# Kernel tuning notes

Hardware: AMD Instinct MI355X
Metric: run time of the kernel (lower is better)

The kernel has to match this reference:

```python
import jax, jax.numpy as jnp
import numpy as np

N = 100000   # nodes
E = 1600000  # edges
D = 128      # feature dim
G = 64       # graphs in batch


def setup_inputs() -> dict:
    key = jax.random.key(0)
    k1, k2, k3, k4, k5, k6, k7, k8 = jax.random.split(key, 8)
    in_feat = jax.random.normal(k1, (N, D), dtype=jnp.float32)
    src = jax.random.randint(k2, (E,), 0, N, dtype=jnp.int32)
    dst = jax.random.randint(k3, (E,), 0, N, dtype=jnp.int32)
    graph_ids = jax.random.randint(k4, (N,), 0, G, dtype=jnp.int32)
    s = 1.0 / np.sqrt(D)
    W1 = jax.random.uniform(k5, (D, D), jnp.float32, -s, s)
    b1 = jnp.zeros((D,), jnp.float32)
    W2 = jax.random.uniform(k6, (D, D), jnp.float32, -s, s)
    b2 = jnp.zeros((D,), jnp.float32)
    return {"in_feat": in_feat, "W1": W1, "b1": b1, "W2": W2, "b2": b2,
            "src": src, "dst": dst, "graph_ids": graph_ids}


def _graph_conv(x, src, dst, W, b, norm_src, norm_dst):
    # DGL GraphConv, norm='both': D_out^{-1/2} A D_in^{-1/2} X W + b
    m = (x * norm_src[:, None])[src]                       # [E, d] gather
    agg = jax.ops.segment_sum(m, dst, num_segments=N)      # [N, d] scatter-add
    return (agg * norm_dst[:, None]) @ W + b


def reference(in_feat, W1, b1, W2, b2, src, dst, graph_ids):
    ones_e = jnp.ones((E,), jnp.float32)
    deg_out = jax.ops.segment_sum(ones_e, src, num_segments=N)
    deg_in = jax.ops.segment_sum(ones_e, dst, num_segments=N)
    norm_src = jnp.where(deg_out > 0, deg_out, 1.0) ** -0.5  # D_out^{-1/2}
    norm_dst = jnp.where(deg_in > 0, deg_in, 1.0) ** -0.5    # D_in^{-1/2}

    h = _graph_conv(in_feat, src, dst, W1, b1, norm_src, norm_dst)
    h = jax.nn.relu(h)
    h = _graph_conv(h, src, dst, W2, b2, norm_src, norm_dst)

    # AvgPooling: per-graph mean over nodes -> [G, D]
    sums = jax.ops.segment_sum(h, graph_ids, num_segments=G)
    counts = jax.ops.segment_sum(jnp.ones((N,), jnp.float32), graph_ids, num_segments=G)
    return sums / jnp.maximum(counts, 1.0)[:, None]
```

## Files before the change

### kernel.cpp

```cpp
#include <hip/hip_runtime.h>
#include <cstdint>


#define DD 128
#define PB 512
#define GB 384
#define KC 32
#define CHK 3200

typedef __attribute__((ext_vector_type(8))) short bf16x8;
typedef __attribute__((ext_vector_type(4))) float f32x4;
typedef __attribute__((ext_vector_type(2))) float f32x2;

__device__ __forceinline__ unsigned short f2bf(float f) {
  union { float f; unsigned u; } v; v.f = f;
  unsigned r = (v.u + 0x7fff + ((v.u >> 16) & 1)) >> 16;
  return (unsigned short)r;
}
__device__ __forceinline__ float bfhi(unsigned u) {
  union { unsigned u; float f; } v; v.u = u & 0xffff0000u; return v.f;
}
__device__ __forceinline__ float bflo(unsigned u) {
  union { unsigned u; float f; } v; v.u = u << 16; return v.f;
}
__device__ __forceinline__ unsigned char f2fp8(float f) {
  return (unsigned char)(__builtin_amdgcn_cvt_pk_fp8_f32(f, f, 0, false) & 0xff);
}

__global__ __launch_bounds__(256) void k_part1a(const int* __restrict__ src, const int* __restrict__ dst,
                                                const int* __restrict__ gid,
                                                unsigned* __restrict__ histD, unsigned* __restrict__ histS,
                                                int* __restrict__ gcnt, int E, int N, int G) {
  __shared__ unsigned hD[256], hS[256];
  __shared__ int h64[64];
  hD[threadIdx.x] = 0; hS[threadIdx.x] = 0;
  if (threadIdx.x < 64) h64[threadIdx.x] = 0;
  __syncthreads();
  int chunk = (E + gridDim.x - 1) / gridDim.x;
  int e0 = blockIdx.x * chunk, e1 = min(E, e0 + chunk);
  for (int e = e0 + threadIdx.x; e < e1; e += 256) {
    atomicAdd(&hD[(unsigned)dst[e] >> 9], 1u);
    atomicAdd(&hS[(unsigned)src[e] >> 9], 1u);
  }
  int stride = gridDim.x * 256;
  for (int i = blockIdx.x * 256 + threadIdx.x; i < N; i += stride)
    atomicAdd(&h64[gid[i]], 1);
  __syncthreads();
  histD[blockIdx.x * 256 + threadIdx.x] = hD[threadIdx.x];
  histS[blockIdx.x * 256 + threadIdx.x] = hS[threadIdx.x];
  if (threadIdx.x < (unsigned)G) {
    int v = h64[threadIdx.x];
    if (v) atomicAdd(&gcnt[threadIdx.x], v);
  }
}

__global__ __launch_bounds__(256) void k_pscanA(unsigned* __restrict__ histD, unsigned* __restrict__ histS,
                                                unsigned* __restrict__ tot) {
  __shared__ unsigned excl[PB], psc[256];
  int table = blockIdx.x >> 8, b = blockIdx.x & 255;
  unsigned* hist = table ? histS : histD;
  int t = threadIdx.x;
  unsigned s0 = hist[(2 * t) * 256 + b];
  unsigned s1 = hist[(2 * t + 1) * 256 + b];
  unsigned pr = s0 + s1;
  psc[t] = pr;
  __syncthreads();
  for (int off = 1; off < 256; off <<= 1) {
    unsigned x = (t >= off) ? psc[t - off] : 0;
    __syncthreads();
    psc[t] += x;
    __syncthreads();
  }
  unsigned pex = psc[t] - pr;
  excl[2 * t] = pex;
  excl[2 * t + 1] = pex + s0;
  __syncthreads();
  hist[(2 * t) * 256 + b] = excl[2 * t];
  hist[(2 * t + 1) * 256 + b] = excl[2 * t + 1];
  if (t == 255) tot[table * 256 + b] = psc[255];
}

__global__ __launch_bounds__(256) void k_pscanB(const unsigned* __restrict__ tot,
                                                int* __restrict__ bsD, int* __restrict__ bsS) {
  __shared__ unsigned s[256];
  int t = threadIdx.x;
#pragma unroll
  for (int table = 0; table < 2; ++table) {
    int* bs = table ? bsS : bsD;
    unsigned v = tot[table * 256 + t];
    s[t] = v;
    __syncthreads();
    for (int off = 1; off < 256; off <<= 1) {
      unsigned x = (t >= off) ? s[t - off] : 0;
      __syncthreads();
      s[t] += x;
      __syncthreads();
    }
    bs[t] = (int)(s[t] - v);
    if (t == 255) bs[256] = (int)s[255];
    __syncthreads();
  }
}

__global__ __launch_bounds__(256) void k_pscanC(unsigned* __restrict__ histD, unsigned* __restrict__ histS,
                                                const int* __restrict__ bsD, const int* __restrict__ bsS) {
  int table = blockIdx.x >> 9, i = blockIdx.x & (PB - 1);
  unsigned* hist = table ? histS : histD;
  const int* bs = table ? bsS : bsD;
  hist[i * 256 + threadIdx.x] += (unsigned)bs[threadIdx.x];
}

__global__ __launch_bounds__(256) void k_part1c(const int* __restrict__ src, const int* __restrict__ dst,
                                                const unsigned* __restrict__ histD, const unsigned* __restrict__ histS,
                                                unsigned* __restrict__ pairD, unsigned* __restrict__ pairS, int E) {
  __shared__ unsigned pk[CHK];
  __shared__ unsigned char bk[CHK];
  __shared__ unsigned hist[256], cur[256], gbase[256], psc[256];
  int chunk = (E + gridDim.x - 1) / gridDim.x;
  int e0 = blockIdx.x * chunk, e1 = min(E, e0 + chunk);
  int n = e1 - e0;
  int t = threadIdx.x;
#pragma unroll
  for (int table = 0; table < 2; ++table) {
    const unsigned* gcur = (table ? histS : histD) + blockIdx.x * 256;
    unsigned* out = table ? pairS : pairD;
    hist[t] = 0;
    __syncthreads();
    for (int i = t; i < n; i += 256) {
      unsigned key = (unsigned)(table ? src[e0 + i] : dst[e0 + i]);
      atomicAdd(&hist[key >> 9], 1u);
    }
    __syncthreads();
    unsigned v = hist[t];
    psc[t] = v;
    __syncthreads();
    for (int off = 1; off < 256; off <<= 1) {
      unsigned x = (t >= off) ? psc[t - off] : 0;
      __syncthreads();
      psc[t] += x;
      __syncthreads();
    }
    unsigned excl = psc[t] - v;
    cur[t] = excl;
    gbase[t] = gcur[t] - excl;
    __syncthreads();
    for (int i = t; i < n; i += 256) {
      unsigned sv = (unsigned)src[e0 + i], dv = (unsigned)dst[e0 + i];
      unsigned key = table ? sv : dv;
      unsigned val = table ? (((sv & 511u) << 17) | dv) : (((dv & 511u) << 17) | sv);
      unsigned b = key >> 9;
      unsigned p = atomicAdd(&cur[b], 1u);
      pk[p] = val;
      bk[p] = (unsigned char)b;
    }
    __syncthreads();
    for (int i = t; i < n; i += 256)
      out[gbase[bk[i]] + i] = pk[i];
    __syncthreads();
  }
}

__global__ __launch_bounds__(256) void k_part2d(const unsigned* __restrict__ pairD, const int* __restrict__ bsD,
                                                int* __restrict__ offs, int* __restrict__ degI,
                                                int* __restrict__ srcS, int N) {
  __shared__ unsigned hist[512], excl[512], psc[256];
  int k = blockIdx.x, base = k << 9;
  int b0 = bsD[k], b1 = bsD[k + 1];
  hist[threadIdx.x] = 0; hist[threadIdx.x + 256] = 0;
  __syncthreads();
  for (int i = b0 + threadIdx.x; i < b1; i += 256)
    atomicAdd(&hist[pairD[i] >> 17], 1u);
  __syncthreads();
  unsigned s0 = hist[2 * threadIdx.x], s1 = hist[2 * threadIdx.x + 1];
  unsigned pr = s0 + s1;
  psc[threadIdx.x] = pr;
  __syncthreads();
  for (int off = 1; off < 256; off <<= 1) {
    unsigned x = (threadIdx.x >= off) ? psc[threadIdx.x - off] : 0;
    __syncthreads();
    psc[threadIdx.x] += x;
    __syncthreads();
  }
  unsigned pex = psc[threadIdx.x] - pr;
  excl[2 * threadIdx.x] = pex;
  excl[2 * threadIdx.x + 1] = pex + s0;
  __syncthreads();
  for (int j = threadIdx.x; j < 512; j += 256) {
    int node = base + j;
    if (node <= N) offs[node] = b0 + (int)excl[j];
    if (node < N) degI[node] = (int)hist[j];
  }
  __syncthreads();
  for (int i = b0 + threadIdx.x; i < b1; i += 256) {
    unsigned pkv = pairD[i];
    unsigned pos = atomicAdd(&excl[pkv >> 17], 1u);
    srcS[b0 + (int)pos] = (int)(pkv & 0x1FFFFu);
  }
}

__global__ __launch_bounds__(256) void k_norm(const int* __restrict__ degI, const int* __restrict__ gcnt,
                                              const int* __restrict__ gid,
                                              float* __restrict__ ndst, uint2* __restrict__ pwg, int N) {
  int i = blockIdx.x * blockDim.x + threadIdx.x;
  if (i >= N) return;
  float gi = (float)degI[i]; gi = gi > 0.f ? gi : 1.f;
  float nd = rsqrtf(gi);
  ndst[i] = nd;
  float c = (float)gcnt[gid[i]]; c = c > 1.f ? c : 1.f;
  float w = nd / c;
  union { float f; unsigned u; } v; v.f = w;
  pwg[i] = make_uint2(v.u, (unsigned)gid[i]);
}

__global__ __launch_bounds__(1024, 1) void k_pw(const unsigned* __restrict__ pairS, const int* __restrict__ bsS,
                                                const uint2* __restrict__ pwg,
                                                unsigned short* __restrict__ P16,
                                                float* __restrict__ nsrc, int N) {
  __shared__ float tile[512 * 64];
  __shared__ unsigned hist[512];
  int k = blockIdx.x, base = k << 9;
  int b0 = bsS[k], b1 = bsS[k + 1];
  for (int i = threadIdx.x; i < 512 * 64; i += 1024) tile[i] = 0.f;
  if (threadIdx.x < 512) hist[threadIdx.x] = 0;
  __syncthreads();
  for (int i = b0 + threadIdx.x; i < b1; i += 1024) {
    unsigned pkv = pairS[i];
    unsigned dv = pkv & 0x1FFFFu;
    unsigned sloc = pkv >> 17;
    atomicAdd(&hist[sloc], 1u);
    uint2 u = pwg[dv];
    union { unsigned u; float f; } w; w.u = u.x;
    atomicAdd(&tile[sloc * 64 + u.y], w.f);
  }
  __syncthreads();
  if (threadIdx.x < 512) {
    int node = base + threadIdx.x;
    if (node < N) {
      float g = (float)hist[threadIdx.x]; g = g > 0.f ? g : 1.f;
      nsrc[node] = rsqrtf(g);
    }
  }
  for (int grp = threadIdx.x; grp < 4096; grp += 1024) {
    int qb = grp >> 6, g = grp & 63;
    unsigned w0 = (unsigned)f2bf(tile[(qb * 8 + 0) * 64 + g]) | ((unsigned)f2bf(tile[(qb * 8 + 1) * 64 + g]) << 16);
    unsigned w1 = (unsigned)f2bf(tile[(qb * 8 + 2) * 64 + g]) | ((unsigned)f2bf(tile[(qb * 8 + 3) * 64 + g]) << 16);
    unsigned w2 = (unsigned)f2bf(tile[(qb * 8 + 4) * 64 + g]) | ((unsigned)f2bf(tile[(qb * 8 + 5) * 64 + g]) << 16);
    unsigned w3 = (unsigned)f2bf(tile[(qb * 8 + 6) * 64 + g]) | ((unsigned)f2bf(tile[(qb * 8 + 7) * 64 + g]) << 16);
    uint4 o = make_uint4(w0, w1, w2, w3);
    *(uint4*)(P16 + ((size_t)(base >> 3) + qb) * 512 + g * 8) = o;
  }
}

__global__ __launch_bounds__(128) void k_wprep(const float* __restrict__ W, unsigned short* __restrict__ Wt) {
  int n = blockIdx.x, k = threadIdx.x;
  Wt[n * 128 + k] = f2bf(W[k * 128 + n]);
}

__global__ __launch_bounds__(256) void k_gemm1(const float* __restrict__ X, const unsigned short* __restrict__ Wt,
                                               const float* __restrict__ nsrc,
                                               unsigned char* __restrict__ Z8, int N) {
  int wave = threadIdx.x >> 6, lane = threadIdx.x & 63;
  int quad = lane >> 4, l16 = lane & 15;
  int row0 = blockIdx.x * 64 + wave * 16;
  int arow = row0 + l16; if (arow >= N) arow = N - 1;
  const float* xr = X + (size_t)arow * 128 + quad * 8;
  f32x4 acc[8];
#pragma unroll
  for (int i = 0; i < 8; ++i) acc[i] = (f32x4){0.f, 0.f, 0.f, 0.f};
#pragma unroll
  for (int kb = 0; kb < 128; kb += 32) {
    float4 x0 = *(const float4*)(xr + kb);
    float4 x1 = *(const float4*)(xr + kb + 4);
    bf16x8 a;
    a[0] = (short)f2bf(x0.x); a[1] = (short)f2bf(x0.y);
    a[2] = (short)f2bf(x0.z); a[3] = (short)f2bf(x0.w);
    a[4] = (short)f2bf(x1.x); a[5] = (short)f2bf(x1.y);
    a[6] = (short)f2bf(x1.z); a[7] = (short)f2bf(x1.w);
#pragma unroll
    for (int nt = 0; nt < 8; ++nt) {
      bf16x8 b = *(const bf16x8*)(Wt + (size_t)(nt * 16 + l16) * 128 + kb + quad * 8);
      acc[nt] = __builtin_amdgcn_mfma_f32_16x16x32_bf16(a, b, acc[nt], 0, 0, 0);
    }
  }
  int rbase = row0 + quad * 4;
#pragma unroll
  for (int r = 0; r < 4; ++r) {
    int row = rbase + r;
    if (row < N) {
      float s = nsrc[row];
#pragma unroll
      for (int nt = 0; nt < 8; ++nt)
        Z8[(size_t)row * 128 + nt * 16 + l16] = f2fp8(acc[nt][r] * s);
    }
  }
}

__global__ __launch_bounds__(256) void k_layer1(const unsigned char* __restrict__ Z8,
                                                const int* __restrict__ offs, const int* __restrict__ srcS,
                                                const float* __restrict__ b1,
                                                const float* __restrict__ nsrc, const float* __restrict__ ndst,
                                                unsigned short* __restrict__ Hb, int N) {
  int lane = threadIdx.x & 63;
  int half = lane >> 5, l32 = lane & 31;
  int d = blockIdx.x * 4 + (threadIdx.x >> 6);
  if (d >= N) return;
  int start = offs[d], end = offs[d + 1];
  float a0 = 0.f, a1 = 0.f, a2 = 0.f, a3 = 0.f;
  int e = start;
  for (; e + 8 <= end; e += 8) {
    int s0 = srcS[e + half], s1 = srcS[e + 2 + half];
    int s2 = srcS[e + 4 + half], s3 = srcS[e + 6 + half];
    unsigned u0 = *(const unsigned*)(Z8 + (size_t)s0 * 128 + l32 * 4);
    unsigned u1 = *(const unsigned*)(Z8 + (size_t)s1 * 128 + l32 * 4);
    unsigned u2 = *(const unsigned*)(Z8 + (size_t)s2 * 128 + l32 * 4);
    unsigned u3 = *(const unsigned*)(Z8 + (size_t)s3 * 128 + l32 * 4);
    f32x2 p0 = __builtin_amdgcn_cvt_pk_f32_fp8(u0, false), q0 = __builtin_amdgcn_cvt_pk_f32_fp8(u0, true);
    f32x2 p1 = __builtin_amdgcn_cvt_pk_f32_fp8(u1, false), q1 = __builtin_amdgcn_cvt_pk_f32_fp8(u1, true);
    f32x2 p2 = __builtin_amdgcn_cvt_pk_f32_fp8(u2, false), q2 = __builtin_amdgcn_cvt_pk_f32_fp8(u2, true);
    f32x2 p3 = __builtin_amdgcn_cvt_pk_f32_fp8(u3, false), q3 = __builtin_amdgcn_cvt_pk_f32_fp8(u3, true);
    a0 += (p0[0] + p1[0]) + (p2[0] + p3[0]);
    a1 += (p0[1] + p1[1]) + (p2[1] + p3[1]);
    a2 += (q0[0] + q1[0]) + (q2[0] + q3[0]);
    a3 += (q0[1] + q1[1]) + (q2[1] + q3[1]);
  }
  for (; e + 2 <= end; e += 2) {
    int s = srcS[e + half];
    unsigned u = *(const unsigned*)(Z8 + (size_t)s * 128 + l32 * 4);
    f32x2 p = __builtin_amdgcn_cvt_pk_f32_fp8(u, false), q = __builtin_amdgcn_cvt_pk_f32_fp8(u, true);
    a0 += p[0]; a1 += p[1]; a2 += q[0]; a3 += q[1];
  }
  if (e < end && half == 0) {
    int s = srcS[e];
    unsigned u = *(const unsigned*)(Z8 + (size_t)s * 128 + l32 * 4);
    f32x2 p = __builtin_amdgcn_cvt_pk_f32_fp8(u, false), q = __builtin_amdgcn_cvt_pk_f32_fp8(u, true);
    a0 += p[0]; a1 += p[1]; a2 += q[0]; a3 += q[1];
  }
  a0 += __shfl_xor(a0, 32, 64);
  a1 += __shfl_xor(a1, 32, 64);
  a2 += __shfl_xor(a2, 32, 64);
  a3 += __shfl_xor(a3, 32, 64);
  if (half == 0) {
    float nd = ndst[d], ns = nsrc[d];
    int f = l32 * 4;
    float h0 = fmaxf(fmaf(nd, a0, b1[f + 0]), 0.f) * ns;
    float h1 = fmaxf(fmaf(nd, a1, b1[f + 1]), 0.f) * ns;
    float h2 = fmaxf(fmaf(nd, a2, b1[f + 2]), 0.f) * ns;
    float h3 = fmaxf(fmaf(nd, a3, b1[f + 3]), 0.f) * ns;
    ushort4 o; o.x = f2bf(h0); o.y = f2bf(h1); o.z = f2bf(h2); o.w = f2bf(h3);
    *(ushort4*)(Hb + (size_t)d * 128 + f) = o;
  }
}

__global__ __launch_bounds__(256) void k_poolgemm(const unsigned short* __restrict__ P16,
                                                  const unsigned short* __restrict__ Hb,
                                                  float* __restrict__ part, int N, int Kpad, int chunk) {
  __shared__ unsigned short Hl[KC * 128];
  int t = threadIdx.x;
  int r0 = blockIdx.x * chunk;
  int r1 = min(Kpad, r0 + chunk);
  int wv = t >> 6, lane = t & 63, quad = lane >> 4, l16 = lane & 15;
  f32x4 acc[8];
#pragma unroll
  for (int i = 0; i < 8; ++i) acc[i] = (f32x4){0.f, 0.f, 0.f, 0.f};
  for (int rb = r0; rb < r1; rb += KC) {
    int r = t >> 3, c = (t & 7) * 16;
    int cs = c ^ ((r >> 3) * 16);
    int row = rb + r;
    if (row < N) {
      const uint4* srcp = (const uint4*)(Hb + (size_t)row * 128 + c);
      *(uint4*)(Hl + r * 128 + cs) = srcp[0];
      *(uint4*)(Hl + r * 128 + cs + 8) = srcp[1];
    } else {
      uint4 z = make_uint4(0, 0, 0, 0);
      *(uint4*)(Hl + r * 128 + cs) = z;
      *(uint4*)(Hl + r * 128 + cs + 8) = z;
    }
    __syncthreads();
    bf16x8 a = *(const bf16x8*)(P16 + ((size_t)(rb >> 3) + quad) * 512 + (wv * 16 + l16) * 8);
#pragma unroll
    for (int ft = 0; ft < 8; ++ft) {
      bf16x8 b;
#pragma unroll
      for (int j = 0; j < 8; ++j) {
        int rr = quad * 8 + j;
        b[j] = (short)Hl[rr * 128 + ((ft ^ (rr >> 3)) * 16) + l16];
      }
      acc[ft] = __builtin_amdgcn_mfma_f32_16x16x32_bf16(a, b, acc[ft], 0, 0, 0);
    }
    __syncthreads();
  }
  float* bp = part + (size_t)blockIdx.x * 64 * DD;
#pragma unroll
  for (int ft = 0; ft < 8; ++ft)
#pragma unroll
    for (int rg = 0; rg < 4; ++rg)
      bp[(wv * 16 + quad * 4 + rg) * DD + ft * 16 + l16] = acc[ft][rg];
}

__global__ __launch_bounds__(256) void k_fold(const float* __restrict__ part, float* __restrict__ pooled) {
  int tid = blockIdx.x * 256 + threadIdx.x;
  int o = tid & 8191, grp = tid >> 13;
  float s = 0.f;
  for (int k = grp; k < GB; k += 8) s += part[(size_t)k * 8192 + o];
  unsafeAtomicAdd(&pooled[o], s);
}

__global__ __launch_bounds__(128) void k_out(const float* __restrict__ pooled, const float* __restrict__ W2,
                                             const float* __restrict__ b2, float* __restrict__ out) {
  __shared__ float p[DD];
  int g = blockIdx.x, d = threadIdx.x;
  p[d] = pooled[g * DD + d];
  __syncthreads();
  float a = b2[d];
#pragma unroll 4
  for (int k = 0; k < DD; ++k) a = fmaf(p[k], W2[k * DD + d], a);
  out[g * DD + d] = a;
}

extern "C" void kernel_launch(void* const* d_in, const int* in_sizes, int n_in,
                              void* d_out, int out_size, void* d_ws, size_t ws_size,
                              hipStream_t stream) {
  const float* X  = (const float*)d_in[0];
  const float* W1 = (const float*)d_in[1];
  const float* b1 = (const float*)d_in[2];
  const float* W2 = (const float*)d_in[3];
  const float* b2 = (const float*)d_in[4];
  const int* src  = (const int*)d_in[5];
  const int* dst  = (const int*)d_in[6];
  const int* gid  = (const int*)d_in[7];
  int E = in_sizes[5];
  int N = in_sizes[7];
  int G = out_size / DD;
  int nb = (N >> 9) + 1;
  int Kpad = nb << 9;
  int chunk = ((Kpad + GB * KC - 1) / (GB * KC)) * KC;

  char* w = (char*)d_ws;
  size_t o = 0;
  auto carve = [&](size_t bytes) { char* p = w + o; o += (bytes + 255) & ~(size_t)255; return p; };
  int*   gcnt   = (int*)  carve((size_t)G * 4);
  float* pooled = (float*)carve((size_t)G * DD * 4);
  size_t zeroBytes = o;
  unsigned* histD = (unsigned*)carve((size_t)PB * 256 * 4);
  unsigned* histS = (unsigned*)carve((size_t)PB * 256 * 4);
  unsigned* tot   = (unsigned*)carve(512 * 4);
  int*   bsD    = (int*)  carve(257 * 4);
  int*   bsS    = (int*)  carve(257 * 4);
  unsigned* pairD = (unsigned*)carve((size_t)E * 4);
  unsigned* pairS = (unsigned*)carve((size_t)E * 4);
  int*   srcS   = (int*)  carve((size_t)E * 4);
  int*   offs   = (int*)  carve((size_t)(N + 1) * 4);
  int*   degI   = (int*)  carve((size_t)N * 4);
  float* nsrc   = (float*)carve((size_t)N * 4);
  float* ndst   = (float*)carve((size_t)N * 4);
  uint2* pwg    = (uint2*)carve((size_t)N * 8);
  unsigned short* Wt = (unsigned short*)carve(128 * 128 * 2);
  unsigned char*  Z8 = (unsigned char*)carve((size_t)N * DD);
  unsigned short* Hb = (unsigned short*)carve((size_t)N * DD * 2);
  unsigned short* P16 = (unsigned short*)carve((size_t)Kpad * 64 * 2);
  float* part   = (float*)pairD;

  hipMemsetAsync(d_ws, 0, zeroBytes, stream);

  k_part1a<<<PB, 256, 0, stream>>>(src, dst, gid, histD, histS, gcnt, E, N, G);
  k_pscanA<<<512, 256, 0, stream>>>(histD, histS, tot);
  k_pscanB<<<1, 256, 0, stream>>>(tot, bsD, bsS);
  k_pscanC<<<2 * PB, 256, 0, stream>>>(histD, histS, bsD, bsS);
  k_part1c<<<PB, 256, 0, stream>>>(src, dst, histD, histS, pairD, pairS, E);
  k_part2d<<<nb, 256, 0, stream>>>(pairD, bsD, offs, degI, srcS, N);
  k_norm<<<(N + 255) / 256, 256, 0, stream>>>(degI, gcnt, gid, ndst, pwg, N);
  k_pw<<<nb, 1024, 0, stream>>>(pairS, bsS, pwg, P16, nsrc, N);
  k_wprep<<<128, 128, 0, stream>>>(W1, Wt);
  k_gemm1<<<(N + 63) / 64, 256, 0, stream>>>(X, Wt, nsrc, Z8, N);
  k_layer1<<<(N + 3) / 4, 256, 0, stream>>>(Z8, offs, srcS, b1, nsrc, ndst, Hb, N);
  k_poolgemm<<<GB, 256, 0, stream>>>(P16, Hb, part, N, Kpad, chunk);
  k_fold<<<256, 256, 0, stream>>>(part, pooled);
  k_out<<<G, DD, 0, stream>>>(pooled, W2, b2, (float*)d_out);
}
```

Measured before the change: 312.9 us.

## Map four destination nodes per wavefront with 8-byte gathers in layer-1 aggregation

The layer-1 aggregation kernel now gives each 16-lane quarter-wave its own destination node, and each lane loads 8 fp8 features (uint2) per neighbor. Before, one node used a whole wave split into two halves and ended with a cross-half shuffle reduction. Source indices for the next pair of edges are prefetched while the current pair is accumulated, with packed f32x2 accumulators. This removes idle lanes on low-degree nodes and the shuffle step, but nodes of different degree now share a wave, which adds divergence through the __any loop.

```diff
diff --git a/kernel.cpp b/kernel.cpp
--- a/kernel.cpp
+++ b/kernel.cpp
@@ -295,59 +295,63 @@
   }
 }
 
+#define ACCP(u) do {                                              \
+    c0 += __builtin_amdgcn_cvt_pk_f32_fp8((u).x, false);          \
+    c1 += __builtin_amdgcn_cvt_pk_f32_fp8((u).x, true);           \
+    c2 += __builtin_amdgcn_cvt_pk_f32_fp8((u).y, false);          \
+    c3 += __builtin_amdgcn_cvt_pk_f32_fp8((u).y, true);           \
+  } while (0)
+
 __global__ __launch_bounds__(256) void k_layer1(const unsigned char* __restrict__ Z8,
                                                 const int* __restrict__ offs, const int* __restrict__ srcS,
                                                 const float* __restrict__ b1,
                                                 const float* __restrict__ nsrc, const float* __restrict__ ndst,
                                                 unsigned short* __restrict__ Hb, int N) {
   int lane = threadIdx.x & 63;
-  int half = lane >> 5, l32 = lane & 31;
-  int d = blockIdx.x * 4 + (threadIdx.x >> 6);
-  if (d >= N) return;
-  int start = offs[d], end = offs[d + 1];
-  float a0 = 0.f, a1 = 0.f, a2 = 0.f, a3 = 0.f;
+  int q = lane >> 4, l16 = lane & 15;
+  int d = blockIdx.x * 16 + (threadIdx.x >> 6) * 4 + q;
+  bool live = d < N;
+  int dc = live ? d : N - 1;
+  int start = offs[dc];
+  int end = live ? offs[dc + 1] : start;
+  const int boff = l16 * 8;
+  const unsigned char* zb = Z8 + boff;
+  float4 bv0 = *(const float4*)(b1 + boff);
+  float4 bv1 = *(const float4*)(b1 + boff + 4);
+  float nd = ndst[dc], ns = nsrc[dc];
+  f32x2 c0 = {0.f, 0.f}, c1 = {0.f, 0.f}, c2 = {0.f, 0.f}, c3 = {0.f, 0.f};
   int e = start;
-  for (; e + 8 <= end; e += 8) {
-    int s0 = srcS[e + half], s1 = srcS[e + 2 + half];
-    int s2 = srcS[e + 4 + half], s3 = srcS[e + 6 + half];
-    unsigned u0 = *(const unsigned*)(Z8 + (size_t)s0 * 128 + l32 * 4);
-    unsigned u1 = *(const unsigned*)(Z8 + (size_t)s1 * 128 + l32 * 4);
-    unsigned u2 = *(const unsigned*)(Z8 + (size_t)s2 * 128 + l32 * 4);
-    unsigned u3 = *(const unsigned*)(Z8 + (size_t)s3 * 128 + l32 * 4);
-    f32x2 p0 = __builtin_amdgcn_cvt_pk_f32_fp8(u0, false), q0 = __builtin_amdgcn_cvt_pk_f32_fp8(u0, true);
-    f32x2 p1 = __builtin_amdgcn_cvt_pk_f32_fp8(u1, false), q1 = __builtin_amdgcn_cvt_pk_f32_fp8(u1, true);
-    f32x2 p2 = __builtin_amdgcn_cvt_pk_f32_fp8(u2, false), q2 = __builtin_amdgcn_cvt_pk_f32_fp8(u2, true);
-    f32x2 p3 = __builtin_amdgcn_cvt_pk_f32_fp8(u3, false), q3 = __builtin_amdgcn_cvt_pk_f32_fp8(u3, true);
-    a0 += (p0[0] + p1[0]) + (p2[0] + p3[0]);
-    a1 += (p0[1] + p1[1]) + (p2[1] + p3[1]);
-    a2 += (q0[0] + q1[0]) + (q2[0] + q3[0]);
-    a3 += (q0[1] + q1[1]) + (q2[1] + q3[1]);
-  }
-  for (; e + 2 <= end; e += 2) {
-    int s = srcS[e + half];
-    unsigned u = *(const unsigned*)(Z8 + (size_t)s * 128 + l32 * 4);
-    f32x2 p = __builtin_amdgcn_cvt_pk_f32_fp8(u, false), q = __builtin_amdgcn_cvt_pk_f32_fp8(u, true);
-    a0 += p[0]; a1 += p[1]; a2 += q[0]; a3 += q[1];
-  }
-  if (e < end && half == 0) {
-    int s = srcS[e];
-    unsigned u = *(const unsigned*)(Z8 + (size_t)s * 128 + l32 * 4);
-    f32x2 p = __builtin_amdgcn_cvt_pk_f32_fp8(u, false), q = __builtin_amdgcn_cvt_pk_f32_fp8(u, true);
-    a0 += p[0]; a1 += p[1]; a2 += q[0]; a3 += q[1];
-  }
-  a0 += __shfl_xor(a0, 32, 64);
-  a1 += __shfl_xor(a1, 32, 64);
-  a2 += __shfl_xor(a2, 32, 64);
-  a3 += __shfl_xor(a3, 32, 64);
-  if (half == 0) {
-    float nd = ndst[d], ns = nsrc[d];
-    int f = l32 * 4;
-    float h0 = fmaxf(fmaf(nd, a0, b1[f + 0]), 0.f) * ns;
-    float h1 = fmaxf(fmaf(nd, a1, b1[f + 1]), 0.f) * ns;
-    float h2 = fmaxf(fmaf(nd, a2, b1[f + 2]), 0.f) * ns;
-    float h3 = fmaxf(fmaf(nd, a3, b1[f + 3]), 0.f) * ns;
-    ushort4 o; o.x = f2bf(h0); o.y = f2bf(h1); o.z = f2bf(h2); o.w = f2bf(h3);
-    *(ushort4*)(Hb + (size_t)d * 128 + f) = o;
+  int rem = end - start;
+  int s0 = (rem > 0) ? srcS[e] : 0;
+  int s1 = (rem > 1) ? srcS[e + 1] : 0;
+  while (__any(rem > 0)) {
+    uint2 u0 = make_uint2(0u, 0u), u1 = make_uint2(0u, 0u);
+    if (rem > 0) u0 = *(const uint2*)(zb + ((size_t)s0 << 7));
+    if (rem > 1) u1 = *(const uint2*)(zb + ((size_t)s1 << 7));
+    int rem2 = rem - 2;
+    if (rem2 > 0) {
+      s0 = srcS[e + 2];
+      if (rem2 > 1) s1 = srcS[e + 3];
+    }
+    ACCP(u0);
+    ACCP(u1);
+    e += 2;
+    rem = rem2;
+  }
+  if (live) {
+    float h0 = fmaxf(fmaf(nd, c0[0], bv0.x), 0.f) * ns;
+    float h1 = fmaxf(fmaf(nd, c0[1], bv0.y), 0.f) * ns;
+    float h2 = fmaxf(fmaf(nd, c1[0], bv0.z), 0.f) * ns;
+    float h3 = fmaxf(fmaf(nd, c1[1], bv0.w), 0.f) * ns;
+    float h4 = fmaxf(fmaf(nd, c2[0], bv1.x), 0.f) * ns;
+    float h5 = fmaxf(fmaf(nd, c2[1], bv1.y), 0.f) * ns;
+    float h6 = fmaxf(fmaf(nd, c3[0], bv1.z), 0.f) * ns;
+    float h7 = fmaxf(fmaf(nd, c3[1], bv1.w), 0.f) * ns;
+    unsigned w0 = (unsigned)f2bf(h0) | ((unsigned)f2bf(h1) << 16);
+    unsigned w1 = (unsigned)f2bf(h2) | ((unsigned)f2bf(h3) << 16);
+    unsigned w2 = (unsigned)f2bf(h4) | ((unsigned)f2bf(h5) << 16);
+    unsigned w3 = (unsigned)f2bf(h6) | ((unsigned)f2bf(h7) << 16);
+    *(uint4*)(Hb + (size_t)d * 128 + boff) = make_uint4(w0, w1, w2, w3);
   }
 }
 
@@ -472,7 +476,7 @@
   k_pw<<<nb, 1024, 0, stream>>>(pairS, bsS, pwg, P16, nsrc, N);
   k_wprep<<<128, 128, 0, stream>>>(W1, Wt);
   k_gemm1<<<(N + 63) / 64, 256, 0, stream>>>(X, Wt, nsrc, Z8, N);
-  k_layer1<<<(N + 3) / 4, 256, 0, stream>>>(Z8, offs, srcS, b1, nsrc, ndst, Hb, N);
+  k_layer1<<<(N + 15) / 16, 256, 0, stream>>>(Z8, offs, srcS, b1, nsrc, ndst, Hb, N);
   k_poolgemm<<<GB, 256, 0, stream>>>(P16, Hb, part, N, Kpad, chunk);
   k_fold<<<256, 256, 0, stream>>>(part, pooled);
   k_out<<<G, DD, 0, stream>>>(pooled, W2, b2, (float*)d_out);
```

New measurement: 298.7 us. -4.5%, faster.
